# Optimization experiments

Measured on AMD Instinct MI355X. Metric: run time of the kernel, lower is better.

## Reference

```python
import jax, jax.numpy as jnp
import numpy as np

B, T, D = 32, 4096, 768          # docs, BERT tokens per doc, feat_dim
MAX_DOC_LEN = 64                 # clauses per doc
MAX_CLAUSE_LEN = 64              # tokens per clause (64*64 == T)
NEG_FILL = -900000.0             # same constant as masked_fill_ in the torch code


def setup_inputs() -> dict:
    key = jax.random.key(0)
    k1, k2, k3, k4 = jax.random.split(key, 4)
    hidden_states = jax.random.normal(k1, (B, T, D), dtype=jnp.float32)
    # ragged clause lengths in [1, MAX_CLAUSE_LEN]; cumulative sum <= T by construction
    clause_len = jax.random.randint(k2, (B, MAX_DOC_LEN), 1, MAX_CLAUSE_LEN + 1, dtype=jnp.int32)
    fc_w = jax.random.normal(k3, (D,), dtype=jnp.float32) * 0.02
    fc_b = jnp.zeros((1,), dtype=jnp.float32)
    emo_w = jax.random.normal(k4, (D,), dtype=jnp.float32) * 0.02
    emo_b = jnp.zeros((1,), dtype=jnp.float32)
    return {"hidden_states": hidden_states, "clause_len": clause_len,
            "fc_w": fc_w, "fc_b": fc_b, "emo_w": emo_w, "emo_b": emo_b}


def reference(hidden_states, clause_len, fc_w, fc_b, emo_w, emo_b):
    # --- get_sentence_state: ragged gather of clauses into [B, J, K, D] + token mask ---
    starts = jnp.cumsum(clause_len, axis=1) - clause_len            # exclusive cumsum [B, J]
    tok = jnp.arange(MAX_CLAUSE_LEN, dtype=jnp.int32)               # [K]
    idx = starts[:, :, None] + tok[None, None, :]                   # [B, J, K] token positions
    valid = tok[None, None, :] < clause_len[:, :, None]             # [B, J, K] mask_doc
    idx = jnp.clip(idx, 0, T - 1)
    flat = idx.reshape(B, MAX_DOC_LEN * MAX_CLAUSE_LEN)
    gathered = jnp.take_along_axis(hidden_states, flat[:, :, None], axis=1)
    sent = gathered.reshape(B, MAX_DOC_LEN, MAX_CLAUSE_LEN, D)
    sent = jnp.where(valid[..., None], sent, 0.0)                   # zero-pad like torch.cat with zeros

    # --- bert_encoder pooling: alpha = fc(h); masked_fill(-9e5); softmax over tokens; weighted sum ---
    alpha = jnp.einsum('bjkd,d->bjk', sent, fc_w) + fc_b[0]
    alpha = jnp.where(valid, alpha, NEG_FILL)
    alpha = jax.nn.softmax(alpha, axis=-1)
    doc_sents_h = jnp.einsum('bjk,bjkd->bjd', alpha, sent)          # [B, J, D]

    # --- pred_emo head ---
    pred_emo = jax.nn.sigmoid(jnp.einsum('bjd,d->bj', doc_sents_h, emo_w) + emo_b[0])
    return pred_emo
```

## Files before the change

kernel.cpp:

```cpp
#include <hip/hip_runtime.h>

#define NB 32
#define TT 4096
#define DD 768
#define NJ 64
#define NK 64

__global__ __launch_bounds__(256) void clause_pool_kernel(
    const float* __restrict__ hs,
    const int*   __restrict__ clause_len,
    const float* __restrict__ fc_w,
    const float* __restrict__ fc_b,
    const float* __restrict__ emo_w,
    const float* __restrict__ emo_b,
    float*       __restrict__ out)
{
    const int bj   = blockIdx.x;
    const int b    = bj >> 6;
    const int j    = bj & 63;
    const int tid  = threadIdx.x;
    const int lane = tid & 63;
    const int wave = tid >> 6;

    const float4* fw4 = (const float4*)fc_w;
    const float4* ew4 = (const float4*)emo_w;
    const float4 wf0 = fw4[lane], wf1 = fw4[lane + 64], wf2 = fw4[lane + 128];
    const float4 we0 = ew4[lane], we1 = ew4[lane + 64], we2 = ew4[lane + 128];

    const int cl   = clause_len[(b << 6) + lane];
    const int clen = __shfl(cl, j, 64);
    int pre = (lane < j) ? cl : 0;
    #pragma unroll
    for (int s = 1; s < 64; s <<= 1) pre += __shfl_xor(pre, s, 64);
    const int start = pre;

    __shared__ float sfc[NK];
    __shared__ float sem[NK];

    const float* base = hs + ((size_t)b * TT + (size_t)start) * DD;

    for (int k = wave; k < clen; k += 4) {
        const float4* row = (const float4*)(base + (size_t)k * DD);
        const float4 h0 = row[lane];
        const float4 h1 = row[lane + 64];
        const float4 h2 = row[lane + 128];

        float pf = h0.x * wf0.x;
        pf = fmaf(h0.y, wf0.y, pf); pf = fmaf(h0.z, wf0.z, pf); pf = fmaf(h0.w, wf0.w, pf);
        pf = fmaf(h1.x, wf1.x, pf); pf = fmaf(h1.y, wf1.y, pf);
        pf = fmaf(h1.z, wf1.z, pf); pf = fmaf(h1.w, wf1.w, pf);
        pf = fmaf(h2.x, wf2.x, pf); pf = fmaf(h2.y, wf2.y, pf);
        pf = fmaf(h2.z, wf2.z, pf); pf = fmaf(h2.w, wf2.w, pf);

        float pe = h0.x * we0.x;
        pe = fmaf(h0.y, we0.y, pe); pe = fmaf(h0.z, we0.z, pe); pe = fmaf(h0.w, we0.w, pe);
        pe = fmaf(h1.x, we1.x, pe); pe = fmaf(h1.y, we1.y, pe);
        pe = fmaf(h1.z, we1.z, pe); pe = fmaf(h1.w, we1.w, pe);
        pe = fmaf(h2.x, we2.x, pe); pe = fmaf(h2.y, we2.y, pe);
        pe = fmaf(h2.z, we2.z, pe); pe = fmaf(h2.w, we2.w, pe);

        #pragma unroll
        for (int s = 1; s < 64; s <<= 1) {
            pf += __shfl_xor(pf, s, 64);
            pe += __shfl_xor(pe, s, 64);
        }
        if (lane == 0) { sfc[k] = pf; sem[k] = pe; }
    }
    __syncthreads();

    if (wave == 0) {
        const float fcb = fc_b[0];
        const bool valid = lane < clen;
        float v = valid ? (sfc[lane] + fcb) : -3.0e38f;
        float m = v;
        #pragma unroll
        for (int s = 1; s < 64; s <<= 1) m = fmaxf(m, __shfl_xor(m, s, 64));
        const float e  = valid ? __expf(v - m) : 0.0f;
        const float ws = valid ? (e * sem[lane]) : 0.0f;
        float Z = e, S = ws;
        #pragma unroll
        for (int s = 1; s < 64; s <<= 1) {
            Z += __shfl_xor(Z, s, 64);
            S += __shfl_xor(S, s, 64);
        }
        if (lane == 0) {
            const float logit = S / Z + emo_b[0];
            out[bj] = 1.0f / (1.0f + __expf(-logit));
        }
    }
}

extern "C" void kernel_launch(void* const* d_in, const int* in_sizes, int n_in,
                              void* d_out, int out_size, void* d_ws, size_t ws_size,
                              hipStream_t stream) {
    const float* hs         = (const float*)d_in[0];
    const int*   clause_len = (const int*)d_in[1];
    const float* fc_w       = (const float*)d_in[2];
    const float* fc_b       = (const float*)d_in[3];
    const float* emo_w      = (const float*)d_in[4];
    const float* emo_b      = (const float*)d_in[5];
    float* out = (float*)d_out;

    clause_pool_kernel<<<NB * NJ, 256, 0, stream>>>(
        hs, clause_len, fc_w, fc_b, emo_w, emo_b, out);
}
```

Measured before the change: 40.68 us.

## Split clause pooling into uniform per-token dot kernel and per-clause softmax kernel

```diff
diff --git a/kernel.cpp b/kernel.cpp
--- a/kernel.cpp
+++ b/kernel.cpp
@@ -5,42 +5,41 @@
 #define DD 768
 #define NJ 64
 #define NK 64
+#define NCLAUSES (NB * NJ)
 
-__global__ __launch_bounds__(256) void clause_pool_kernel(
+#define ROWS_PER_CHUNK 32
+#define CHUNKS_PER_DOC (TT / ROWS_PER_CHUNK)
+
+__global__ __launch_bounds__(256) void dots_kernel(
     const float* __restrict__ hs,
     const int*   __restrict__ clause_len,
     const float* __restrict__ fc_w,
-    const float* __restrict__ fc_b,
     const float* __restrict__ emo_w,
-    const float* __restrict__ emo_b,
-    float*       __restrict__ out)
+    float*       __restrict__ ws_fc,
+    float*       __restrict__ ws_emo)
 {
-    const int bj   = blockIdx.x;
-    const int b    = bj >> 6;
-    const int j    = bj & 63;
-    const int tid  = threadIdx.x;
-    const int lane = tid & 63;
-    const int wave = tid >> 6;
+    const int b     = blockIdx.x >> 7;
+    const int chunk = blockIdx.x & (CHUNKS_PER_DOC - 1);
+    const int lane  = threadIdx.x & 63;
+    const int wave  = threadIdx.x >> 6;
+
+    int L = clause_len[(b << 6) + lane];
+    #pragma unroll
+    for (int s = 1; s < 64; s <<= 1) L += __shfl_xor(L, s, 64);
+
+    const int base = chunk * ROWS_PER_CHUNK;
+    if (base + wave >= L) return;
 
     const float4* fw4 = (const float4*)fc_w;
     const float4* ew4 = (const float4*)emo_w;
     const float4 wf0 = fw4[lane], wf1 = fw4[lane + 64], wf2 = fw4[lane + 128];
     const float4 we0 = ew4[lane], we1 = ew4[lane + 64], we2 = ew4[lane + 128];
 
-    const int cl   = clause_len[(b << 6) + lane];
-    const int clen = __shfl(cl, j, 64);
-    int pre = (lane < j) ? cl : 0;
-    #pragma unroll
-    for (int s = 1; s < 64; s <<= 1) pre += __shfl_xor(pre, s, 64);
-    const int start = pre;
+    for (int i = 0; i < 8; ++i) {
+        const int t = base + (i << 2) + wave;
+        if (t >= L) break;
 
-    __shared__ float sfc[NK];
-    __shared__ float sem[NK];
-
-    const float* base = hs + ((size_t)b * TT + (size_t)start) * DD;
-
-    for (int k = wave; k < clen; k += 4) {
-        const float4* row = (const float4*)(base + (size_t)k * DD);
+        const float4* row = (const float4*)(hs + ((size_t)b * TT + t) * DD);
         const float4 h0 = row[lane];
         const float4 h1 = row[lane + 64];
         const float4 h2 = row[lane + 128];
@@ -64,29 +63,54 @@
             pf += __shfl_xor(pf, s, 64);
             pe += __shfl_xor(pe, s, 64);
         }
-        if (lane == 0) { sfc[k] = pf; sem[k] = pe; }
+        if (lane == 0) {
+            ws_fc [b * TT + t] = pf;
+            ws_emo[b * TT + t] = pe;
+        }
     }
-    __syncthreads();
+}
 
-    if (wave == 0) {
-        const float fcb = fc_b[0];
-        const bool valid = lane < clen;
-        float v = valid ? (sfc[lane] + fcb) : -3.0e38f;
-        float m = v;
-        #pragma unroll
-        for (int s = 1; s < 64; s <<= 1) m = fmaxf(m, __shfl_xor(m, s, 64));
-        const float e  = valid ? __expf(v - m) : 0.0f;
-        const float ws = valid ? (e * sem[lane]) : 0.0f;
-        float Z = e, S = ws;
-        #pragma unroll
-        for (int s = 1; s < 64; s <<= 1) {
-            Z += __shfl_xor(Z, s, 64);
-            S += __shfl_xor(S, s, 64);
-        }
-        if (lane == 0) {
-            const float logit = S / Z + emo_b[0];
-            out[bj] = 1.0f / (1.0f + __expf(-logit));
-        }
+__global__ __launch_bounds__(256) void pool_kernel(
+    const int*   __restrict__ clause_len,
+    const float* __restrict__ ws_fc,
+    const float* __restrict__ ws_emo,
+    const float* __restrict__ fc_b,
+    const float* __restrict__ emo_b,
+    float*       __restrict__ out)
+{
+    const int lane = threadIdx.x & 63;
+    const int wave = threadIdx.x >> 6;
+    const int bj   = (blockIdx.x << 2) + wave;
+    const int b    = bj >> 6;
+    const int j    = bj & 63;
+
+    const int cl   = clause_len[(b << 6) + lane];
+    const int clen = __shfl(cl, j, 64);
+    int pre = (lane < j) ? cl : 0;
+    #pragma unroll
+    for (int s = 1; s < 64; s <<= 1) pre += __shfl_xor(pre, s, 64);
+    const int start = pre;
+
+    const bool valid = lane < clen;
+    const int  t     = start + lane;
+    const float sfc  = valid ? ws_fc [b * TT + t] : 0.0f;
+    const float sem  = valid ? ws_emo[b * TT + t] : 0.0f;
+
+    float v = valid ? (sfc + fc_b[0]) : -3.0e38f;
+    float m = v;
+    #pragma unroll
+    for (int s = 1; s < 64; s <<= 1) m = fmaxf(m, __shfl_xor(m, s, 64));
+    const float e  = valid ? __expf(v - m) : 0.0f;
+    const float wsum = e * sem;
+    float Z = e, S = wsum;
+    #pragma unroll
+    for (int s = 1; s < 64; s <<= 1) {
+        Z += __shfl_xor(Z, s, 64);
+        S += __shfl_xor(S, s, 64);
+    }
+    if (lane == 0) {
+        const float logit = S / Z + emo_b[0];
+        out[bj] = 1.0f / (1.0f + __expf(-logit));
     }
 }
 
@@ -101,6 +125,11 @@
     const float* emo_b      = (const float*)d_in[5];
     float* out = (float*)d_out;
 
-    clause_pool_kernel<<<NB * NJ, 256, 0, stream>>>(
-        hs, clause_len, fc_w, fc_b, emo_w, emo_b, out);
+    float* ws_fc  = (float*)d_ws;
+    float* ws_emo = ws_fc + NB * TT;
+
+    dots_kernel<<<NB * CHUNKS_PER_DOC, 256, 0, stream>>>(
+        hs, clause_len, fc_w, emo_w, ws_fc, ws_emo);
+    pool_kernel<<<NCLAUSES / 4, 256, 0, stream>>>(
+        clause_len, ws_fc, ws_emo, fc_b, emo_b, out);
 }
```

New measurement: 40.17 us. Within noise of the previous version (-1.3%).
